# Kernel tuning notes

Hardware: AMD Instinct MI355X
Metric: run time of the kernel (lower is better)

Reference implementation:

```python
import jax, jax.numpy as jnp
import numpy as np

_EPS = 1e-5
RC = 5.0   # cutoff radius
L = 20     # number of radial basis functions
N = 10000  # nodes
E = 100000 # edges
F = 128    # in_feats


def _ssp(x):
    # ShiftedSoftplus: softplus(x) - log(2)
    return jax.nn.softplus(x) - jnp.log(2.0)


def _rbf(r):
    # DimeNet radial basis: sqrt(2/rc) * sin(n*pi*r/rc) / r, n = 1..L.  r: [E,1] -> [E,L]
    n = jnp.arange(1, L + 1, dtype=r.dtype)
    return jnp.sqrt(2.0 / RC) * jnp.sin(n * jnp.pi * r / RC) / r


def _fc(u):
    # cosine cutoff applied elementwise: 0.5*(cos(pi*u/rc)+1) for u < rc else 0
    return jnp.where(u < RC, 0.5 * (jnp.cos(jnp.pi * u / RC) + 1.0), 0.0)


def setup_inputs() -> dict:
    key = jax.random.key(0)
    ks = jax.random.split(key, 12)

    def nrm(k, shape, scale=1.0):
        return jax.random.normal(k, shape, dtype=jnp.float32) * scale

    return {
        "x": nrm(ks[0], (N, 3)) * 3.0,           # atomic positions
        "v": nrm(ks[1], (N, F, 3)),               # vector node features
        "s": nrm(ks[2], (N, F)),                  # scalar node features
        "ms1_w": nrm(ks[3], (F, F), F ** -0.5),
        "ms1_b": jnp.zeros((F,), jnp.float32),
        "ms2_w": nrm(ks[4], (3 * F, F), F ** -0.5),
        "ms2_b": jnp.zeros((3 * F,), jnp.float32),
        "mv_w": nrm(ks[5], (3 * F, L), L ** -0.5),
        "mv_b": jnp.zeros((3 * F,), jnp.float32),
        "us1_w": nrm(ks[6], (F, F), F ** -0.5),
        "us1_b": jnp.zeros((F,), jnp.float32),
        "us2_w": nrm(ks[7], (3 * F, F), F ** -0.5),
        "us2_b": jnp.zeros((3 * F,), jnp.float32),
        "src": jax.random.randint(ks[8], (E,), 0, N, dtype=jnp.int32),
        "dst": jax.random.randint(ks[9], (E,), 0, N, dtype=jnp.int32),
    }


def reference(x, v, s, ms1_w, ms1_b, ms2_w, ms2_b, mv_w, mv_b,
              us1_w, us1_b, us2_w, us2_b, src, dst):
    # ---------- pass 1: message1 + reduce1 (sum over incoming edges) ----------
    sj = s[src]                                   # [E,F]   src scalar features
    vj = v[src]                                   # [E,F,3] src vector features
    vec = x[src] - x[dst]                         # [E,3]   x_i - x_j (molecule branch)
    r = jnp.sqrt(jnp.sum(vec ** 2, axis=-1) + _EPS)[:, None]          # [E,1]
    phi = _ssp(sj @ ms1_w.T + ms1_b) @ ms2_w.T + ms2_b                 # [E,3F]
    w = _fc(_rbf(r) @ mv_w.T + mv_b)                                    # [E,3F]
    v_, s_, r_ = jnp.split(phi * w, 3, axis=-1)                         # each [E,F]
    dv_e = vj * v_[:, :, None] + r_[:, :, None] * (vec / r)[:, None, :] # [E,F,3]
    dv = jax.ops.segment_sum(dv_e, dst, num_segments=N)                 # [N,F,3]
    ds = jax.ops.segment_sum(s_, dst, num_segments=N)                   # [N,F]
    v_new = v + dv
    s_new = s + ds

    # ---------- pass 2: message2 + reduce2 (mean over incoming edges) ----------
    s2 = _ssp(s_new[src] @ us1_w.T + us1_b) @ us2_w.T + us2_b           # [E,3F]
    deg = jax.ops.segment_sum(jnp.ones((E,), s.dtype), dst, num_segments=N)
    denom = jnp.maximum(deg, 1.0)
    s_mean = jax.ops.segment_sum(s2, dst, num_segments=N) / denom[:, None]        # [N,3F]
    uv = jax.ops.segment_sum(v_new[src], dst, num_segments=N) / denom[:, None, None]  # [N,F,3]
    avv, asv, ass = jnp.split(s_mean, 3, axis=-1)                       # each [N,F]
    norm = jnp.sqrt(jnp.sum(uv ** 2, axis=-1) + _EPS)[..., None]        # [N,F,1]
    dv2 = uv * avv[:, :, None]                                           # [N,F,3]
    ds2 = jnp.sum((uv / norm) ** 2, axis=-1) * asv + ass                 # [N,F]
    return (v_new + dv2, s_new + ds2)
```

## Files before the change

### kernel.cpp

```cpp
#include <hip/hip_runtime.h>
#include <hip/hip_bf16.h>


#define F_DIM   128
#define F3_DIM  384
#define L_DIM   20
#define CAP     64
#define BATCH   16

typedef __attribute__((ext_vector_type(8))) short short8;
typedef __attribute__((ext_vector_type(4))) float f32x4;
typedef __attribute__((ext_vector_type(4))) unsigned short us4;

struct u3 { unsigned a, b, c; };

__device__ __forceinline__ unsigned short f2bf(float f) {
  union { float f; unsigned u; } a; a.f = f;
  unsigned u = a.u;
  u = (u + 0x7FFFu + ((u >> 16) & 1u)) >> 16;
  return (unsigned short)u;
}
__device__ __forceinline__ float bf2f(unsigned short u) {
  union { unsigned u; float f; } a; a.u = ((unsigned)u) << 16;
  return a.f;
}

__global__ __launch_bounds__(256) void cast_fill_kernel(
    const float* __restrict__ ms1_w, unsigned short* __restrict__ w_ms1,
    const float* __restrict__ ms2_w, unsigned short* __restrict__ w_ms2,
    const float* __restrict__ us1_w, unsigned short* __restrict__ w_us1,
    const float* __restrict__ us2_w, unsigned short* __restrict__ w_us2,
    const float* __restrict__ s,     unsigned short* __restrict__ sbf,
    const float* __restrict__ v,     us4* __restrict__ v4,
    const float* __restrict__ mv_w,  unsigned short* __restrict__ mvwB,
    const int* __restrict__ src, const int* __restrict__ dst,
    int* __restrict__ cursor, int* __restrict__ jbuf,
    int nF, int E)
{
  int i = blockIdx.x * 256 + threadIdx.x;
  if (i < 16384) w_ms1[i] = f2bf(ms1_w[i]);
  if (i < 49152) w_ms2[i] = f2bf(ms2_w[i]);
  if (i < 16384) w_us1[i] = f2bf(us1_w[i]);
  if (i < 49152) w_us2[i] = f2bf(us2_w[i]);
  if (i < nF)    sbf[i] = f2bf(s[i]);
  if (i < nF) {
    const float* vp = v + (size_t)i * 3;
    us4 o; o.x = f2bf(vp[0]); o.y = f2bf(vp[1]); o.z = f2bf(vp[2]); o.w = 0;
    v4[i] = o;
  }
  if (i < 384 * 32) {
    int o = i >> 5, k = i & 31;
    float val = (k < 20) ? mv_w[o * 20 + k] * 0.6324555320336759f : 0.f;
    mvwB[i] = f2bf(val);
  }
  if (i < E) {
    int d = dst[i];
    int p = atomicAdd(&cursor[d], 1);
    if (p < CAP) jbuf[d * CAP + p] = src[i];
  }
}

__global__ __launch_bounds__(64) void mlp_kernel(
    const unsigned short* __restrict__ X,
    const unsigned short* __restrict__ W1,
    const float* __restrict__ B1,
    const unsigned short* __restrict__ W2,
    const float* __restrict__ B2,
    const us4* __restrict__ Vin,
    unsigned short* __restrict__ Yc)
{
  __shared__ float HT[128 * 17];
  const int lane = threadIdx.x;
  const int c    = lane & 15;
  const int quad = lane >> 4;
  const int m0   = blockIdx.x * 16;

  f32x4 acc[8];
#pragma unroll
  for (int t = 0; t < 8; t++) acc[t] = (f32x4){0.f, 0.f, 0.f, 0.f};
#pragma unroll
  for (int kk = 0; kk < 4; kk++) {
    short8 a = *(const short8*)(X + (size_t)(m0 + c) * 128 + kk * 32 + quad * 8);
#pragma unroll
    for (int t = 0; t < 8; t++) {
      short8 b = *(const short8*)(W1 + (size_t)(t * 16 + c) * 128 + kk * 32 + quad * 8);
      acc[t] = __builtin_amdgcn_mfma_f32_16x16x32_bf16(a, b, acc[t], 0, 0, 0);
    }
  }
#pragma unroll
  for (int t = 0; t < 8; t++) {
    float bias = B1[t * 16 + c];
    int k = t * 16 + c;
#pragma unroll
    for (int r = 0; r < 4; r++) {
      float h = acc[t][r] + bias;
      float sp = (h > 15.f) ? h : log1pf(__expf(h));
      sp -= 0.69314718056f;
      HT[k * 17 + quad * 4 + r] = sp;
    }
  }
  __syncthreads();

  f32x4 acc2[3][8];
#pragma unroll
  for (int g = 0; g < 3; g++)
#pragma unroll
    for (int t = 0; t < 8; t++) acc2[g][t] = (f32x4){0.f, 0.f, 0.f, 0.f};
#pragma unroll
  for (int kk = 0; kk < 4; kk++) {
    short8 afr;
#pragma unroll
    for (int j = 0; j < 8; j++) {
      float hv = HT[(kk * 32 + quad * 8 + j) * 17 + c];
      afr[j] = (short)f2bf(hv);
    }
#pragma unroll
    for (int g = 0; g < 3; g++)
#pragma unroll
      for (int t = 0; t < 8; t++) {
        short8 b = *(const short8*)(W2 + (size_t)(g * 128 + t * 16 + c) * 128 + kk * 32 + quad * 8);
        acc2[g][t] = __builtin_amdgcn_mfma_f32_16x16x32_bf16(afr, b, acc2[g][t], 0, 0, 0);
      }
  }
#pragma unroll
  for (int t = 0; t < 8; t++) {
    int f = t * 16 + c;
    float b0 = B2[f], b1 = B2[128 + f], b2 = B2[256 + f];
#pragma unroll
    for (int r = 0; r < 4; r++) {
      int m = quad * 4 + r;
      us4 vv = Vin[(size_t)(m0 + m) * 128 + f];
      unsigned p0 = f2bf(acc2[0][t][r] + b0);
      unsigned p1 = f2bf(acc2[1][t][r] + b1);
      unsigned p2 = f2bf(acc2[2][t][r] + b2);
      u3 rec;
      rec.a = p0 | (p1 << 16);
      rec.b = p2 | ((unsigned)vv.x << 16);
      rec.c = (unsigned)vv.y | ((unsigned)vv.z << 16);
      *(u3*)(Yc + ((size_t)(m0 + m) * 128 + f) * 6) = rec;
    }
  }
}

__global__ __launch_bounds__(256, 4) void pass1_kernel(
    const float* __restrict__ x,
    const unsigned short* __restrict__ combo1,
    const float* __restrict__ v,
    const float* __restrict__ s,
    const unsigned short* __restrict__ mvwB,
    const float* __restrict__ mv_b,
    const int* __restrict__ jbuf,
    const int* __restrict__ deg,
    float* __restrict__ vnew, us4* __restrict__ vnew4,
    float* __restrict__ snew, unsigned short* __restrict__ snew_bf, int nNodes)
{
  __shared__ unsigned short Asn[BATCH * 32];
  __shared__ float4 Au[BATCH];
  __shared__ us4 Wl[BATCH * 128];
  __shared__ float red[512];

  const int tid  = threadIdx.x;
  const int wave = tid >> 6, lane = tid & 63;
  const int half = wave >> 1, split = wave & 1;
  const int i = blockIdx.x;
  const int f = lane + 64 * half;
  const int c = lane & 15, quad = lane >> 4;

  int cnt = deg[i]; if (cnt > CAP) cnt = CAP;
  const int base = i * CAP;

  short8 bfr[6]; float bias[6];
#pragma unroll
  for (int p = 0; p < 3; p++)
#pragma unroll
    for (int h = 0; h < 2; h++) {
      int t = 2 * wave + h + 8 * p;
      bfr[p * 2 + h]  = *(const short8*)(mvwB + (size_t)(t * 16 + c) * 32 + quad * 8);
      bias[p * 2 + h] = mv_b[t * 16 + c];
    }

  const float xi0 = x[i * 3], xi1 = x[i * 3 + 1], xi2 = x[i * 3 + 2];
  int jv = (lane < cnt) ? jbuf[base + lane] : 0;

  float accV0 = 0.f, accV1 = 0.f, accV2 = 0.f, accS = 0.f;

  for (int bs = 0; bs < cnt; bs += BATCH) {
    int bcnt = cnt - bs; if (bcnt > BATCH) bcnt = BATCH;
    __syncthreads();

    if (wave == 0) {
      int t16 = lane & (BATCH - 1);
      int e = bs + t16;
      int j = __shfl(jv, e);
      if (lane < BATCH && e < cnt) {
        float d0 = x[j * 3]     - xi0;
        float d1 = x[j * 3 + 1] - xi1;
        float d2 = x[j * 3 + 2] - xi2;
        float r = sqrtf(d0 * d0 + d1 * d1 + d2 * d2 + 1e-5f);
        float invr = 1.0f / r;
        Au[lane] = make_float4(d0 * invr, d1 * invr, d2 * invr, invr);
        float theta = r * 0.6283185307179586f;
        float s1, c1;
        __sincosf(theta, &s1, &c1);
        float c2 = 2.f * c1;
        float pm2 = s1, pm1 = c2 * s1;
        Asn[lane * 32 + 0] = f2bf(pm2);
        Asn[lane * 32 + 1] = f2bf(pm1);
#pragma unroll
        for (int l = 2; l < L_DIM; l++) {
          float cur = c2 * pm1 - pm2;
          Asn[lane * 32 + l] = f2bf(cur);
          pm2 = pm1; pm1 = cur;
        }
#pragma unroll
        for (int l = L_DIM; l < 32; l++) Asn[lane * 32 + l] = 0;
      }
    }
    __syncthreads();

    {
      short8 a = *(const short8*)&Asn[c * 32 + quad * 8];
      f32x4 acc[6];
#pragma unroll
      for (int q = 0; q < 6; q++)
        acc[q] = __builtin_amdgcn_mfma_f32_16x16x32_bf16(
            a, bfr[q], (f32x4){0.f, 0.f, 0.f, 0.f}, 0, 0, 0);
#pragma unroll
      for (int r = 0; r < 4; r++) {
        int el = quad * 4 + r;
        if (el < bcnt) {
          float invr = Au[el].w;
#pragma unroll
          for (int h = 0; h < 2; h++) {
            float wp0 = fmaf(acc[h][r],     invr, bias[h]);
            float wp1 = fmaf(acc[2 + h][r], invr, bias[2 + h]);
            float wp2 = fmaf(acc[4 + h][r], invr, bias[4 + h]);
            float w0 = (wp0 < 5.f) ? 0.5f * (__cosf(wp0 * 0.6283185307179586f) + 1.f) : 0.f;
            float w1 = (wp1 < 5.f) ? 0.5f * (__cosf(wp1 * 0.6283185307179586f) + 1.f) : 0.f;
            float w2 = (wp2 < 5.f) ? 0.5f * (__cosf(wp2 * 0.6283185307179586f) + 1.f) : 0.f;
            us4 o; o.x = f2bf(w0); o.y = f2bf(w1); o.z = f2bf(w2); o.w = 0;
            Wl[el * 128 + wave * 32 + h * 16 + c] = o;
          }
        }
      }
    }
    __syncthreads();

    u3 cb[8];
    float msk[8];
#pragma unroll
    for (int k = 0; k < 8; k++) {
      int e = split + 2 * k;
      int ec = (e < bcnt) ? e : 0;
      msk[k] = (e < bcnt) ? 1.f : 0.f;
      int j = __shfl(jv, bs + ec);
      cb[k] = *(const u3*)(combo1 + ((size_t)j * 128 + f) * 6);
    }
#pragma unroll
    for (int k = 0; k < 8; k++) {
      int e = split + 2 * k;
      int ec = (e < bcnt) ? e : 0;
      float4 u = Au[ec];
      us4 wv = Wl[ec * 128 + f];
      float ph0 = bf2f((unsigned short)(cb[k].a & 0xffff));
      float ph1 = bf2f((unsigned short)(cb[k].a >> 16));
      float ph2 = bf2f((unsigned short)(cb[k].b & 0xffff));
      float vx  = bf2f((unsigned short)(cb[k].b >> 16));
      float vy  = bf2f((unsigned short)(cb[k].c & 0xffff));
      float vz  = bf2f((unsigned short)(cb[k].c >> 16));
      float m0 = ph0 * bf2f(wv.x) * msk[k];
      float m1 = ph1 * bf2f(wv.y) * msk[k];
      float m2 = ph2 * bf2f(wv.z) * msk[k];
      accV0 = fmaf(vx, m0, fmaf(m2, u.x, accV0));
      accV1 = fmaf(vy, m0, fmaf(m2, u.y, accV1));
      accV2 = fmaf(vz, m0, fmaf(m2, u.z, accV2));
      accS += m1;
    }
  }

  const int idx = half * 64 + lane;
  __syncthreads();
  if (split == 1) {
    red[idx * 4 + 0] = accV0; red[idx * 4 + 1] = accV1;
    red[idx * 4 + 2] = accV2; red[idx * 4 + 3] = accS;
  }
  __syncthreads();
  if (split == 0) {
    accV0 += red[idx * 4 + 0]; accV1 += red[idx * 4 + 1];
    accV2 += red[idx * 4 + 2]; accS  += red[idx * 4 + 3];
    size_t b3 = (size_t)i * 384 + f * 3;
    float n0 = v[b3] + accV0, n1 = v[b3 + 1] + accV1, n2 = v[b3 + 2] + accV2;
    vnew[b3] = n0; vnew[b3 + 1] = n1; vnew[b3 + 2] = n2;
    us4 o; o.x = f2bf(n0); o.y = f2bf(n1); o.z = f2bf(n2); o.w = 0;
    vnew4[(size_t)i * 128 + f] = o;
    size_t b1 = (size_t)i * 128 + f;
    float sv = s[b1] + accS;
    snew[b1] = sv;
    snew_bf[b1] = f2bf(sv);
  }
}

__global__ __launch_bounds__(256, 4) void pass2_kernel(
    const float* __restrict__ vnew,
    const float* __restrict__ snew,
    const unsigned short* __restrict__ combo2,
    const int* __restrict__ jbuf, const int* __restrict__ deg,
    float* __restrict__ vout, float* __restrict__ sout, int nNodes)
{
  __shared__ float red[1024];
  const int wave = threadIdx.x >> 6, lane = threadIdx.x & 63;
  const int half = wave >> 1, split = wave & 1;
  const int i = blockIdx.x;
  const int f = lane + 64 * half;

  int cnt = deg[i]; if (cnt > CAP) cnt = CAP;
  const int base = i * CAP;
  int jv = (lane < cnt) ? jbuf[base + lane] : 0;

  float accU0 = 0.f, accU1 = 0.f, accU2 = 0.f;
  float accM0 = 0.f, accM1 = 0.f, accM2 = 0.f;

  for (int b0 = split; b0 < cnt; b0 += 16) {
    u3 cb[8];
    float msk[8];
#pragma unroll
    for (int k = 0; k < 8; k++) {
      int e = b0 + 2 * k;
      int ec = (e < cnt) ? e : 0;
      msk[k] = (e < cnt) ? 1.f : 0.f;
      int j = __shfl(jv, ec);
      cb[k] = *(const u3*)(combo2 + ((size_t)j * 128 + f) * 6);
    }
#pragma unroll
    for (int k = 0; k < 8; k++) {
      accM0 = fmaf(bf2f((unsigned short)(cb[k].a & 0xffff)), msk[k], accM0);
      accM1 = fmaf(bf2f((unsigned short)(cb[k].a >> 16)),    msk[k], accM1);
      accM2 = fmaf(bf2f((unsigned short)(cb[k].b & 0xffff)), msk[k], accM2);
      accU0 = fmaf(bf2f((unsigned short)(cb[k].b >> 16)),    msk[k], accU0);
      accU1 = fmaf(bf2f((unsigned short)(cb[k].c & 0xffff)), msk[k], accU1);
      accU2 = fmaf(bf2f((unsigned short)(cb[k].c >> 16)),    msk[k], accU2);
    }
  }

  const int idx = half * 64 + lane;
  if (split == 1) {
    red[idx * 8 + 0] = accU0; red[idx * 8 + 1] = accU1; red[idx * 8 + 2] = accU2;
    red[idx * 8 + 3] = accM0; red[idx * 8 + 4] = accM1; red[idx * 8 + 5] = accM2;
  }
  __syncthreads();
  if (split == 0) {
    accU0 += red[idx * 8 + 0]; accU1 += red[idx * 8 + 1]; accU2 += red[idx * 8 + 2];
    accM0 += red[idx * 8 + 3]; accM1 += red[idx * 8 + 4]; accM2 += red[idx * 8 + 5];

    float dinv = 1.0f / (float)(cnt > 0 ? cnt : 1);
    float uv0 = accU0 * dinv, uv1 = accU1 * dinv, uv2 = accU2 * dinv;
    float avv = accM0 * dinv, asv = accM1 * dinv, ass = accM2 * dinv;
    float q = uv0 * uv0 + uv1 * uv1 + uv2 * uv2;
    float ds2 = (q / (q + 1e-5f)) * asv + ass;
    size_t b3 = (size_t)i * 384 + f * 3;
    vout[b3]     = vnew[b3]     + uv0 * avv;
    vout[b3 + 1] = vnew[b3 + 1] + uv1 * avv;
    vout[b3 + 2] = vnew[b3 + 2] + uv2 * avv;
    size_t b1 = (size_t)i * 128 + f;
    sout[b1] = snew[b1] + ds2;
  }
}

extern "C" void kernel_launch(void* const* d_in, const int* in_sizes, int n_in,
                              void* d_out, int out_size, void* d_ws, size_t ws_size,
                              hipStream_t stream)
{
  const float* x     = (const float*)d_in[0];
  const float* v     = (const float*)d_in[1];
  const float* s     = (const float*)d_in[2];
  const float* ms1_w = (const float*)d_in[3];
  const float* ms1_b = (const float*)d_in[4];
  const float* ms2_w = (const float*)d_in[5];
  const float* ms2_b = (const float*)d_in[6];
  const float* mv_w  = (const float*)d_in[7];
  const float* mv_b  = (const float*)d_in[8];
  const float* us1_w = (const float*)d_in[9];
  const float* us1_b = (const float*)d_in[10];
  const float* us2_w = (const float*)d_in[11];
  const float* us2_b = (const float*)d_in[12];
  const int*   src   = (const int*)d_in[13];
  const int*   dst   = (const int*)d_in[14];

  const int N = in_sizes[0] / 3;
  const int E = in_sizes[13];

  char* p = (char*)d_ws;
  auto alloc = [&](size_t bytes) -> void* {
    void* r = (void*)p;
    p += (bytes + 255) & ~(size_t)255;
    return r;
  };
  unsigned short* sbf   = (unsigned short*)alloc((size_t)N * 128 * 2);
  unsigned short* snbf  = (unsigned short*)alloc((size_t)N * 128 * 2);
  unsigned short* w_ms1 = (unsigned short*)alloc(16384 * 2);
  unsigned short* w_ms2 = (unsigned short*)alloc(49152 * 2);
  unsigned short* w_us1 = (unsigned short*)alloc(16384 * 2);
  unsigned short* w_us2 = (unsigned short*)alloc(49152 * 2);
  unsigned short* mvwB  = (unsigned short*)alloc(384 * 32 * 2);
  us4*   v4     = (us4*)alloc((size_t)N * 128 * 8);
  us4*   vnew4  = (us4*)alloc((size_t)N * 128 * 8);
  unsigned short* combo1 = (unsigned short*)alloc((size_t)N * 128 * 12);
  unsigned short* combo2 = (unsigned short*)alloc((size_t)N * 128 * 12);
  float* vnew   = (float*)alloc((size_t)N * 384 * 4);
  float* snew   = (float*)alloc((size_t)N * 128 * 4);
  int* cursor   = (int*)alloc((size_t)N * 4);
  int* jbuf     = (int*)alloc((size_t)N * CAP * 4);

  hipMemsetAsync(cursor, 0, (size_t)N * 4, stream);

  cast_fill_kernel<<<(N * 128 + 255) / 256, 256, 0, stream>>>(
      ms1_w, w_ms1, ms2_w, w_ms2, us1_w, w_us1, us2_w, w_us2,
      s, sbf, v, v4, mv_w, mvwB, src, dst, cursor, jbuf, N * 128, E);

  mlp_kernel<<<N / 16, 64, 0, stream>>>(sbf, w_ms1, ms1_b, w_ms2, ms2_b,
                                        v4, combo1);

  pass1_kernel<<<N, 256, 0, stream>>>(x, combo1, v, s, mvwB, mv_b,
                                      jbuf, cursor, vnew, vnew4, snew, snbf, N);

  mlp_kernel<<<N / 16, 64, 0, stream>>>(snbf, w_us1, us1_b, w_us2, us2_b,
                                        vnew4, combo2);

  float* vout = (float*)d_out;
  float* sout = vout + (size_t)N * 384;
  pass2_kernel<<<N, 256, 0, stream>>>(vnew, snew, combo2, jbuf, cursor,
                                      vout, sout, N);
}
```

Measured before the change: 241.4 us.

## Fuse bf16 casts into MLP loads and simplify pass2 to single-split blocks

The separate bf16 copies of s, v, snew and vnew are dropped. The MLP kernel now reads fp32 inputs and converts them in registers, which removes the cast passes and their intermediate buffers. The cast_fill grid shrinks to cover edges only. Pass1 zero-fills unused edge slots in shared memory so the per-edge masks can go, and pass2 uses 128-thread blocks with no split reduction through shared memory. The trade-off is that the MLP now reads twice as many bytes and does strided fp32 v reads, and pass2 processes edges serially within each thread.

```diff
diff --git a/kernel.cpp b/kernel.cpp
--- a/kernel.cpp
+++ b/kernel.cpp
@@ -30,24 +30,15 @@
     const float* __restrict__ ms2_w, unsigned short* __restrict__ w_ms2,
     const float* __restrict__ us1_w, unsigned short* __restrict__ w_us1,
     const float* __restrict__ us2_w, unsigned short* __restrict__ w_us2,
-    const float* __restrict__ s,     unsigned short* __restrict__ sbf,
-    const float* __restrict__ v,     us4* __restrict__ v4,
     const float* __restrict__ mv_w,  unsigned short* __restrict__ mvwB,
     const int* __restrict__ src, const int* __restrict__ dst,
-    int* __restrict__ cursor, int* __restrict__ jbuf,
-    int nF, int E)
+    int* __restrict__ cursor, int* __restrict__ jbuf, int E)
 {
   int i = blockIdx.x * 256 + threadIdx.x;
   if (i < 16384) w_ms1[i] = f2bf(ms1_w[i]);
   if (i < 49152) w_ms2[i] = f2bf(ms2_w[i]);
   if (i < 16384) w_us1[i] = f2bf(us1_w[i]);
   if (i < 49152) w_us2[i] = f2bf(us2_w[i]);
-  if (i < nF)    sbf[i] = f2bf(s[i]);
-  if (i < nF) {
-    const float* vp = v + (size_t)i * 3;
-    us4 o; o.x = f2bf(vp[0]); o.y = f2bf(vp[1]); o.z = f2bf(vp[2]); o.w = 0;
-    v4[i] = o;
-  }
   if (i < 384 * 32) {
     int o = i >> 5, k = i & 31;
     float val = (k < 20) ? mv_w[o * 20 + k] * 0.6324555320336759f : 0.f;
@@ -61,12 +52,12 @@
 }
 
 __global__ __launch_bounds__(64) void mlp_kernel(
-    const unsigned short* __restrict__ X,
+    const float* __restrict__ X,
     const unsigned short* __restrict__ W1,
     const float* __restrict__ B1,
     const unsigned short* __restrict__ W2,
     const float* __restrict__ B2,
-    const us4* __restrict__ Vin,
+    const float* __restrict__ Vin,
     unsigned short* __restrict__ Yc)
 {
   __shared__ float HT[128 * 17];
@@ -80,7 +71,14 @@
   for (int t = 0; t < 8; t++) acc[t] = (f32x4){0.f, 0.f, 0.f, 0.f};
 #pragma unroll
   for (int kk = 0; kk < 4; kk++) {
-    short8 a = *(const short8*)(X + (size_t)(m0 + c) * 128 + kk * 32 + quad * 8);
+    const float* xp = X + (size_t)(m0 + c) * 128 + kk * 32 + quad * 8;
+    float4 xa = *(const float4*)xp;
+    float4 xb = *(const float4*)(xp + 4);
+    short8 a;
+    a[0] = (short)f2bf(xa.x); a[1] = (short)f2bf(xa.y);
+    a[2] = (short)f2bf(xa.z); a[3] = (short)f2bf(xa.w);
+    a[4] = (short)f2bf(xb.x); a[5] = (short)f2bf(xb.y);
+    a[6] = (short)f2bf(xb.z); a[7] = (short)f2bf(xb.w);
 #pragma unroll
     for (int t = 0; t < 8; t++) {
       short8 b = *(const short8*)(W1 + (size_t)(t * 16 + c) * 128 + kk * 32 + quad * 8);
@@ -129,14 +127,14 @@
 #pragma unroll
     for (int r = 0; r < 4; r++) {
       int m = quad * 4 + r;
-      us4 vv = Vin[(size_t)(m0 + m) * 128 + f];
+      const float* vp = Vin + ((size_t)(m0 + m) * 128 + f) * 3;
       unsigned p0 = f2bf(acc2[0][t][r] + b0);
       unsigned p1 = f2bf(acc2[1][t][r] + b1);
       unsigned p2 = f2bf(acc2[2][t][r] + b2);
       u3 rec;
       rec.a = p0 | (p1 << 16);
-      rec.b = p2 | ((unsigned)vv.x << 16);
-      rec.c = (unsigned)vv.y | ((unsigned)vv.z << 16);
+      rec.b = p2 | ((unsigned)f2bf(vp[0]) << 16);
+      rec.c = (unsigned)f2bf(vp[1]) | ((unsigned)f2bf(vp[2]) << 16);
       *(u3*)(Yc + ((size_t)(m0 + m) * 128 + f) * 6) = rec;
     }
   }
@@ -151,8 +149,7 @@
     const float* __restrict__ mv_b,
     const int* __restrict__ jbuf,
     const int* __restrict__ deg,
-    float* __restrict__ vnew, us4* __restrict__ vnew4,
-    float* __restrict__ snew, unsigned short* __restrict__ snew_bf, int nNodes)
+    float* __restrict__ vnew, float* __restrict__ snew, int nNodes)
 {
   __shared__ unsigned short Asn[BATCH * 32];
   __shared__ float4 Au[BATCH];
@@ -228,49 +225,46 @@
 #pragma unroll
       for (int r = 0; r < 4; r++) {
         int el = quad * 4 + r;
-        if (el < bcnt) {
-          float invr = Au[el].w;
-#pragma unroll
-          for (int h = 0; h < 2; h++) {
+#pragma unroll
+        for (int h = 0; h < 2; h++) {
+          us4 o = (us4){0, 0, 0, 0};
+          if (el < bcnt) {
+            float invr = Au[el].w;
             float wp0 = fmaf(acc[h][r],     invr, bias[h]);
             float wp1 = fmaf(acc[2 + h][r], invr, bias[2 + h]);
             float wp2 = fmaf(acc[4 + h][r], invr, bias[4 + h]);
             float w0 = (wp0 < 5.f) ? 0.5f * (__cosf(wp0 * 0.6283185307179586f) + 1.f) : 0.f;
             float w1 = (wp1 < 5.f) ? 0.5f * (__cosf(wp1 * 0.6283185307179586f) + 1.f) : 0.f;
             float w2 = (wp2 < 5.f) ? 0.5f * (__cosf(wp2 * 0.6283185307179586f) + 1.f) : 0.f;
-            us4 o; o.x = f2bf(w0); o.y = f2bf(w1); o.z = f2bf(w2); o.w = 0;
-            Wl[el * 128 + wave * 32 + h * 16 + c] = o;
+            o.x = f2bf(w0); o.y = f2bf(w1); o.z = f2bf(w2);
           }
+          Wl[el * 128 + wave * 32 + h * 16 + c] = o;
         }
       }
     }
     __syncthreads();
 
     u3 cb[8];
-    float msk[8];
 #pragma unroll
     for (int k = 0; k < 8; k++) {
       int e = split + 2 * k;
-      int ec = (e < bcnt) ? e : 0;
-      msk[k] = (e < bcnt) ? 1.f : 0.f;
-      int j = __shfl(jv, bs + ec);
+      int j = __shfl(jv, bs + e);
       cb[k] = *(const u3*)(combo1 + ((size_t)j * 128 + f) * 6);
     }
 #pragma unroll
     for (int k = 0; k < 8; k++) {
       int e = split + 2 * k;
-      int ec = (e < bcnt) ? e : 0;
-      float4 u = Au[ec];
-      us4 wv = Wl[ec * 128 + f];
+      float4 u = Au[e];
+      us4 wv = Wl[e * 128 + f];
       float ph0 = bf2f((unsigned short)(cb[k].a & 0xffff));
       float ph1 = bf2f((unsigned short)(cb[k].a >> 16));
       float ph2 = bf2f((unsigned short)(cb[k].b & 0xffff));
       float vx  = bf2f((unsigned short)(cb[k].b >> 16));
       float vy  = bf2f((unsigned short)(cb[k].c & 0xffff));
       float vz  = bf2f((unsigned short)(cb[k].c >> 16));
-      float m0 = ph0 * bf2f(wv.x) * msk[k];
-      float m1 = ph1 * bf2f(wv.y) * msk[k];
-      float m2 = ph2 * bf2f(wv.z) * msk[k];
+      float m0 = ph0 * bf2f(wv.x);
+      float m1 = ph1 * bf2f(wv.y);
+      float m2 = ph2 * bf2f(wv.z);
       accV0 = fmaf(vx, m0, fmaf(m2, u.x, accV0));
       accV1 = fmaf(vy, m0, fmaf(m2, u.y, accV1));
       accV2 = fmaf(vz, m0, fmaf(m2, u.z, accV2));
@@ -289,46 +283,39 @@
     accV0 += red[idx * 4 + 0]; accV1 += red[idx * 4 + 1];
     accV2 += red[idx * 4 + 2]; accS  += red[idx * 4 + 3];
     size_t b3 = (size_t)i * 384 + f * 3;
-    float n0 = v[b3] + accV0, n1 = v[b3 + 1] + accV1, n2 = v[b3 + 2] + accV2;
-    vnew[b3] = n0; vnew[b3 + 1] = n1; vnew[b3 + 2] = n2;
-    us4 o; o.x = f2bf(n0); o.y = f2bf(n1); o.z = f2bf(n2); o.w = 0;
-    vnew4[(size_t)i * 128 + f] = o;
+    vnew[b3]     = v[b3]     + accV0;
+    vnew[b3 + 1] = v[b3 + 1] + accV1;
+    vnew[b3 + 2] = v[b3 + 2] + accV2;
     size_t b1 = (size_t)i * 128 + f;
-    float sv = s[b1] + accS;
-    snew[b1] = sv;
-    snew_bf[b1] = f2bf(sv);
-  }
-}
-
-__global__ __launch_bounds__(256, 4) void pass2_kernel(
+    snew[b1] = s[b1] + accS;
+  }
+}
+
+__global__ __launch_bounds__(128, 4) void pass2_kernel(
     const float* __restrict__ vnew,
     const float* __restrict__ snew,
     const unsigned short* __restrict__ combo2,
     const int* __restrict__ jbuf, const int* __restrict__ deg,
     float* __restrict__ vout, float* __restrict__ sout, int nNodes)
 {
-  __shared__ float red[1024];
   const int wave = threadIdx.x >> 6, lane = threadIdx.x & 63;
-  const int half = wave >> 1, split = wave & 1;
   const int i = blockIdx.x;
-  const int f = lane + 64 * half;
+  const int f = lane + 64 * wave;
 
   int cnt = deg[i]; if (cnt > CAP) cnt = CAP;
-  const int base = i * CAP;
-  int jv = (lane < cnt) ? jbuf[base + lane] : 0;
+  int jv = (lane < cnt) ? jbuf[i * CAP + lane] : 0;
 
   float accU0 = 0.f, accU1 = 0.f, accU2 = 0.f;
   float accM0 = 0.f, accM1 = 0.f, accM2 = 0.f;
 
-  for (int b0 = split; b0 < cnt; b0 += 16) {
+  for (int b0 = 0; b0 < cnt; b0 += 8) {
     u3 cb[8];
     float msk[8];
 #pragma unroll
     for (int k = 0; k < 8; k++) {
-      int e = b0 + 2 * k;
-      int ec = (e < cnt) ? e : 0;
+      int e = b0 + k;
       msk[k] = (e < cnt) ? 1.f : 0.f;
-      int j = __shfl(jv, ec);
+      int j = __shfl(jv, e);
       cb[k] = *(const u3*)(combo2 + ((size_t)j * 128 + f) * 6);
     }
 #pragma unroll
@@ -342,28 +329,17 @@
     }
   }
 
-  const int idx = half * 64 + lane;
-  if (split == 1) {
-    red[idx * 8 + 0] = accU0; red[idx * 8 + 1] = accU1; red[idx * 8 + 2] = accU2;
-    red[idx * 8 + 3] = accM0; red[idx * 8 + 4] = accM1; red[idx * 8 + 5] = accM2;
-  }
-  __syncthreads();
-  if (split == 0) {
-    accU0 += red[idx * 8 + 0]; accU1 += red[idx * 8 + 1]; accU2 += red[idx * 8 + 2];
-    accM0 += red[idx * 8 + 3]; accM1 += red[idx * 8 + 4]; accM2 += red[idx * 8 + 5];
-
-    float dinv = 1.0f / (float)(cnt > 0 ? cnt : 1);
-    float uv0 = accU0 * dinv, uv1 = accU1 * dinv, uv2 = accU2 * dinv;
-    float avv = accM0 * dinv, asv = accM1 * dinv, ass = accM2 * dinv;
-    float q = uv0 * uv0 + uv1 * uv1 + uv2 * uv2;
-    float ds2 = (q / (q + 1e-5f)) * asv + ass;
-    size_t b3 = (size_t)i * 384 + f * 3;
-    vout[b3]     = vnew[b3]     + uv0 * avv;
-    vout[b3 + 1] = vnew[b3 + 1] + uv1 * avv;
-    vout[b3 + 2] = vnew[b3 + 2] + uv2 * avv;
-    size_t b1 = (size_t)i * 128 + f;
-    sout[b1] = snew[b1] + ds2;
-  }
+  float dinv = 1.0f / (float)(cnt > 0 ? cnt : 1);
+  float uv0 = accU0 * dinv, uv1 = accU1 * dinv, uv2 = accU2 * dinv;
+  float avv = accM0 * dinv, asv = accM1 * dinv, ass = accM2 * dinv;
+  float q = uv0 * uv0 + uv1 * uv1 + uv2 * uv2;
+  float ds2 = (q / (q + 1e-5f)) * asv + ass;
+  size_t b3 = (size_t)i * 384 + f * 3;
+  vout[b3]     = vnew[b3]     + uv0 * avv;
+  vout[b3 + 1] = vnew[b3 + 1] + uv1 * avv;
+  vout[b3 + 2] = vnew[b3 + 2] + uv2 * avv;
+  size_t b1 = (size_t)i * 128 + f;
+  sout[b1] = snew[b1] + ds2;
 }
 
 extern "C" void kernel_launch(void* const* d_in, const int* in_sizes, int n_in,
@@ -395,15 +371,11 @@
     p += (bytes + 255) & ~(size_t)255;
     return r;
   };
-  unsigned short* sbf   = (unsigned short*)alloc((size_t)N * 128 * 2);
-  unsigned short* snbf  = (unsigned short*)alloc((size_t)N * 128 * 2);
   unsigned short* w_ms1 = (unsigned short*)alloc(16384 * 2);
   unsigned short* w_ms2 = (unsigned short*)alloc(49152 * 2);
   unsigned short* w_us1 = (unsigned short*)alloc(16384 * 2);
   unsigned short* w_us2 = (unsigned short*)alloc(49152 * 2);
   unsigned short* mvwB  = (unsigned short*)alloc(384 * 32 * 2);
-  us4*   v4     = (us4*)alloc((size_t)N * 128 * 8);
-  us4*   vnew4  = (us4*)alloc((size_t)N * 128 * 8);
   unsigned short* combo1 = (unsigned short*)alloc((size_t)N * 128 * 12);
   unsigned short* combo2 = (unsigned short*)alloc((size_t)N * 128 * 12);
   float* vnew   = (float*)alloc((size_t)N * 384 * 4);
@@ -413,21 +385,21 @@
 
   hipMemsetAsync(cursor, 0, (size_t)N * 4, stream);
 
-  cast_fill_kernel<<<(N * 128 + 255) / 256, 256, 0, stream>>>(
+  cast_fill_kernel<<<(E + 255) / 256, 256, 0, stream>>>(
       ms1_w, w_ms1, ms2_w, w_ms2, us1_w, w_us1, us2_w, w_us2,
-      s, sbf, v, v4, mv_w, mvwB, src, dst, cursor, jbuf, N * 128, E);
-
-  mlp_kernel<<<N / 16, 64, 0, stream>>>(sbf, w_ms1, ms1_b, w_ms2, ms2_b,
-                                        v4, combo1);
+      mv_w, mvwB, src, dst, cursor, jbuf, E);
+
+  mlp_kernel<<<N / 16, 64, 0, stream>>>(s, w_ms1, ms1_b, w_ms2, ms2_b,
+                                        v, combo1);
 
   pass1_kernel<<<N, 256, 0, stream>>>(x, combo1, v, s, mvwB, mv_b,
-                                      jbuf, cursor, vnew, vnew4, snew, snbf, N);
-
-  mlp_kernel<<<N / 16, 64, 0, stream>>>(snbf, w_us1, us1_b, w_us2, us2_b,
-                                        vnew4, combo2);
+                                      jbuf, cursor, vnew, snew, N);
+
+  mlp_kernel<<<N / 16, 64, 0, stream>>>(snew, w_us1, us1_b, w_us2, us2_b,
+                                        vnew, combo2);
 
   float* vout = (float*)d_out;
   float* sout = vout + (size_t)N * 384;
-  pass2_kernel<<<N, 256, 0, stream>>>(vnew, snew, combo2, jbuf, cursor,
+  pass2_kernel<<<N, 128, 0, stream>>>(vnew, snew, combo2, jbuf, cursor,
                                       vout, sout, N);
 }
```

After: 242.2 us. No clear change (+0.3%).
